# Kernel tuning notes

Hardware: AMD Instinct MI355X
Metric: run time of the kernel (lower is better)

The kernel has to match this reference:

```python
import jax, jax.numpy as jnp
import numpy as np

B, N, D, H, O, A, L = 128, 100, 2048, 1024, 1600, 400, 2048


def _mlp(x, w1, b1, w2, b2, w3, b3):
    h = jax.nn.relu(x @ w1 + b1)
    h = jax.nn.relu(h @ w2 + b2)
    return jax.nn.softmax(h @ w3 + b3, axis=2)  # softmax over class dim (dim=2)


def setup_inputs() -> dict:
    key = jax.random.key(0)
    ks = jax.random.split(key, 18)

    def lin(kw, fan_in, fan_out):
        s = 1.0 / np.sqrt(fan_in)
        return jax.random.normal(kw, (fan_in, fan_out), jnp.float32) * s

    x = jax.random.normal(ks[0], (B, N, D), jnp.float32)
    num_descs = jax.random.randint(ks[1], (B,), 0, N, jnp.int32)
    label_img = jnp.sort(jax.random.randint(ks[2], (L,), 0, B, jnp.int32))
    obj_labels = jax.random.randint(ks[3], (L,), 0, O)
    att_labels = jax.random.randint(ks[4], (L,), 0, A)

    inp = dict(x=x, num_descs=num_descs, label_img=label_img,
               obj_labels=obj_labels, att_labels=att_labels,
               w1o=lin(ks[5], D, H), b1o=jnp.zeros((H,), jnp.float32),
               w2o=lin(ks[6], H, H), b2o=jnp.zeros((H,), jnp.float32),
               w3o=lin(ks[7], H, O), b3o=jnp.zeros((O,), jnp.float32),
               w1a=lin(ks[8], D, H), b1a=jnp.zeros((H,), jnp.float32),
               w2a=lin(ks[9], H, H), b2a=jnp.zeros((H,), jnp.float32),
               w3a=lin(ks[10], H, A), b3a=jnp.zeros((A,), jnp.float32))
    return inp


def reference(x, num_descs, label_img, obj_labels, att_labels,
              w1o, b1o, w2o, b2o, w3o, b3o,
              w1a, b1a, w2a, b2a, w3a, b3a):
    po = _mlp(x, w1o, b1o, w2o, b2o, w3o, b3o)  # [B, N, O]
    pa = _mlp(x, w1a, b1a, w2a, b2a, w3a, b3a)  # [B, N, A]

    rows = jnp.arange(po.shape[1])  # [N]
    # per-label gather of the prob column for its object/attribute class -> [L, N]
    p_obj = po[label_img[:, None], rows[None, :], obj_labels[:, None]]
    p_att = pa[label_img[:, None], rows[None, :], att_labels[:, None]]
    # ragged unpad (descs beyond num_descs[img] excluded from argmax)
    valid = rows[None, :] < num_descs[label_img][:, None]
    score = jnp.where(valid, p_obj * p_att, -jnp.inf)
    desc = jnp.argmax(score, axis=1)  # [L]

    obj_dists = po[label_img, desc, :]  # [L, O]
    att_dists = pa[label_img, desc, :]  # [L, A]
    return (obj_dists, att_dists)
```

## Files before the change

### kernel.cpp

```cpp
#include <hip/hip_runtime.h>
#include <hip/hip_bf16.h>
#include <math.h>

#define Bq 128
#define Nq 100
#define Dq 2048
#define Hq 1024
#define Oq 1600
#define Aq 400
#define Lq 2048
#define Mq (Bq * Nq)
#define OqP 1664
#define AqP 512

typedef __attribute__((ext_vector_type(8))) short bf16x8;
typedef __attribute__((ext_vector_type(16))) float f32x16;
typedef unsigned short ushort;


__device__ __forceinline__ void split1(float v, ushort& h, ushort& l) {
    __hip_bfloat16 bh = __float2bfloat16(v);
    float fh = __bfloat162float(bh);
    __hip_bfloat16 bl = __float2bfloat16(v - fh);
    h = __builtin_bit_cast(ushort, bh);
    l = __builtin_bit_cast(ushort, bl);
}

__device__ __forceinline__ void gl_lds16(const ushort* g, ushort* lds) {
    __builtin_amdgcn_global_load_lds(
        (const __attribute__((address_space(1))) unsigned int*)g,
        (__attribute__((address_space(3))) unsigned int*)lds,
        16, 0, 0);
}

__global__ void build_offsets(const int* __restrict__ num_descs,
                              int* __restrict__ off, int* __restrict__ mc,
                              int* __restrict__ rowmap)
{
    __shared__ int cnt[Bq];
    __shared__ int offs[Bq + 1];
    const int t = threadIdx.x;
    int nd = num_descs[t];
    nd = nd < 0 ? 0 : (nd > Nq ? Nq : nd);
    const int c = nd < 1 ? 1 : nd;
    cnt[t] = c;
    __syncthreads();
    if (t == 0) {
        int s = 0;
        for (int i = 0; i < Bq; i++) { offs[i] = s; s += cnt[i]; }
        offs[Bq] = s;
        mc[0] = s;
        mc[1] = (s + 127) & ~127;
    }
    __syncthreads();
    off[t] = offs[t];
    for (int i = t; i < Mq; i += Bq) rowmap[i] = -1;
    __syncthreads();
    const int o = offs[t];
    for (int n = 0; n < c; n++) rowmap[o + n] = t * Nq + n;
}

__global__ __launch_bounds__(256) void split_compact(const float* __restrict__ x,
                              const int* __restrict__ rowmap,
                              const int* __restrict__ mc,
                              ushort* __restrict__ hi, ushort* __restrict__ lo)
{
    const int KB = Dq / 16;
    const int nbc = Dq / 64;
    const int rt = blockIdx.x / nbc;
    const int bc = (blockIdx.x - rt * nbc) * 64;
    if (rt * 32 >= mc[1]) return;

    __shared__ float t[32][66];
    const int tid = threadIdx.x;
    {
        const int row = tid >> 3;
        const int coff = (tid & 7) * 8;
        const int crow = rt * 32 + row;
        const int orig = (crow < mc[0]) ? rowmap[crow] : -1;
        float v[8];
        if (orig < 0) {
#pragma unroll
            for (int e = 0; e < 8; e++) v[e] = 0.f;
        } else {
            const float* src = x + (size_t)orig * Dq + bc + coff;
            float4 v0 = *(const float4*)(src);
            float4 v1 = *(const float4*)(src + 4);
            v[0] = v0.x; v[1] = v0.y; v[2] = v0.z; v[3] = v0.w;
            v[4] = v1.x; v[5] = v1.y; v[6] = v1.z; v[7] = v1.w;
        }
#pragma unroll
        for (int e = 0; e < 8; e++) t[row][coff + e] = v[e];
    }
    __syncthreads();

    const int wave = tid >> 6;
    const int lane = tid & 63;
    const int r32 = lane & 31;
    const int cl = wave * 16 + (lane >> 5) * 8;
    ushort h[8], l[8];
#pragma unroll
    for (int e = 0; e < 8; e++) split1(t[r32][cl + e], h[e], l[e]);
    const size_t wid = (size_t)rt * KB + (bc >> 4) + wave;
    const size_t a = wid * 512 + (size_t)lane * 8;
    *(bf16x8*)(hi + a) = *(bf16x8*)h;
    *(bf16x8*)(lo + a) = *(bf16x8*)l;
}

struct TSeg { const float* W; ushort* Th; ushort* Tl; int K; int N; int gx; int base; };
struct TSegs { TSeg s[6]; };

__global__ void tsplit_all(TSegs a)
{
    const int id = blockIdx.x;
    TSeg sg = a.s[5];
#pragma unroll
    for (int i = 4; i >= 0; i--) if (id < a.s[i + 1].base) sg = a.s[i];
    const int local = id - sg.base;
    const int bn = (local % sg.gx) * 32;
    const int bk = (local / sg.gx) * 32;
    const int KB = sg.K >> 4;

    __shared__ float t[32][33];
    const int tx = threadIdx.x & 31, ty = threadIdx.x >> 5;
#pragma unroll
    for (int i = 0; i < 4; i++) {
        const int k = bk + ty + i * 8, n = bn + tx;
        t[ty + i * 8][tx] = (n < sg.N) ? sg.W[(size_t)k * sg.N + n] : 0.f;
    }
    __syncthreads();

    const int wave = threadIdx.x >> 6;
    const int lane = threadIdx.x & 63;
    const int kc = wave & 1;
    const int hl = wave >> 1;
    const int nloc = lane & 31;
    const int kloc = kc * 16 + (lane >> 5) * 8;
    ushort v8[8];
#pragma unroll
    for (int e = 0; e < 8; e++) {
        ushort h, l;
        split1(t[kloc + e][nloc], h, l);
        v8[e] = hl ? l : h;
    }
    const size_t chunk = (size_t)((bn >> 5)) * KB + (bk >> 4) + kc;
    ushort* dst = (hl ? sg.Tl : sg.Th) + chunk * 512 + (size_t)lane * 8;
    *(bf16x8*)dst = *(bf16x8*)v8;
}

struct GArgs {
    const ushort* Ah; const ushort* Al;
    const ushort* Bh; const ushort* Bl;
    const float* bias;
    float* Cf; ushort* Ch; ushort* Cl;
    int K, Npad, Nreal, ldc, mode;
};

__global__ __launch_bounds__(256, 3) void gemm_split(GArgs g0, GArgs g1,
                                                     const int* __restrict__ mcp,
                                                     int nct0, int nct)
{
    const int ny = mcp[1] >> 7;
    const int nact = nct * ny;
    const int hw = blockIdx.x;
    if (hw >= nact) return;
    const int q = nact >> 3, r = nact & 7, xcd = hw & 7, pos = hw >> 3;
    const int L = (xcd < r ? xcd * (q + 1) : r * (q + 1) + (xcd - r) * q) + pos;
    const int by = L / nct;
    const int ct = L - by * nct;

    const GArgs g = (ct < nct0) ? g0 : g1;
    const int bm = by * 128;
    const int bn = (ct < nct0 ? ct : ct - nct0) * 128;

    const int KB = g.K >> 4;

    __shared__ __align__(16) ushort sAh[6144];
    __shared__ __align__(16) ushort sAl[6144];
    __shared__ __align__(16) ushort sBh[6144];
    __shared__ __align__(16) ushort sBl[6144];

    const int tid  = threadIdx.x;
    const int wave = tid >> 6;
    const int lane = tid & 63;
    const int wmi = (wave >> 1) * 2;
    const int wni = (wave & 1) * 2;
    const int l31  = lane & 31;
    const int half = lane >> 5;

    const ushort* gAh = g.Ah + ((size_t)(bm / 32 + wave) * KB) * 512 + lane * 8;
    const ushort* gAl = g.Al + ((size_t)(bm / 32 + wave) * KB) * 512 + lane * 8;
    const ushort* gBh = g.Bh + ((size_t)(bn / 32 + wave) * KB) * 512 + lane * 8;
    const ushort* gBl = g.Bl + ((size_t)(bn / 32 + wave) * KB) * 512 + lane * 8;

    f32x16 acc[2][2] = {};

    auto STAGE = [&](int c) {
        const size_t go = (size_t)c * 512;
        const int ls = (c % 3) * 2048 + (wave << 9);
        gl_lds16(gAh + go, &sAh[ls]);
        gl_lds16(gAl + go, &sAl[ls]);
        gl_lds16(gBh + go, &sBh[ls]);
        gl_lds16(gBl + go, &sBl[ls]);
    };

    auto PHASE = [&](int c, int stage_c, int drain) {
        const int slot = (c % 3) * 2048;
        bf16x8 ah[2], al[2], bh[2], bl[2];
#pragma unroll
        for (int i = 0; i < 2; i++) {
            const int sa = slot + (wmi + i) * 512 + lane * 8;
            const int sb = slot + (wni + i) * 512 + lane * 8;
            ah[i] = *(const bf16x8*)&sAh[sa];
            al[i] = *(const bf16x8*)&sAl[sa];
            bh[i] = *(const bf16x8*)&sBh[sb];
            bl[i] = *(const bf16x8*)&sBl[sb];
        }
        if (stage_c >= 0) STAGE(stage_c);
        __builtin_amdgcn_s_setprio(1);
#pragma unroll
        for (int i = 0; i < 2; i++)
#pragma unroll
            for (int j = 0; j < 2; j++) {
                acc[i][j] = __builtin_amdgcn_mfma_f32_32x32x16_bf16(ah[i], bh[j], acc[i][j], 0, 0, 0);
                acc[i][j] = __builtin_amdgcn_mfma_f32_32x32x16_bf16(ah[i], bl[j], acc[i][j], 0, 0, 0);
                acc[i][j] = __builtin_amdgcn_mfma_f32_32x32x16_bf16(al[i], bh[j], acc[i][j], 0, 0, 0);
            }
        __builtin_amdgcn_s_setprio(0);
        if (drain == 4)      asm volatile("s_waitcnt vmcnt(4)" ::: "memory");
        else if (drain == 0) asm volatile("s_waitcnt vmcnt(0)" ::: "memory");
        if (drain >= 0) {
            asm volatile("s_waitcnt lgkmcnt(0)" ::: "memory");
            asm volatile("s_barrier" ::: "memory");
        }
    };

    STAGE(0); STAGE(1);
    asm volatile("s_waitcnt vmcnt(4)" ::: "memory");
    asm volatile("s_barrier" ::: "memory");

    for (int c = 0; c < KB - 2; ++c) PHASE(c, c + 2, 4);
    PHASE(KB - 2, -1, 0);
    PHASE(KB - 1, -1, -1);

    const int KC = g.ldc >> 4;
#pragma unroll
    for (int j = 0; j < 2; j++) {
        const int col = bn + (wni + j) * 32 + l31;
        if (col < g.Nreal) {
            const float bv = g.bias[col];
#pragma unroll
            for (int i = 0; i < 2; i++) {
#pragma unroll
                for (int r = 0; r < 16; r++) {
                    const int row = bm + (wmi + i) * 32 + (r & 3) + 8 * (r >> 2) + 4 * half;
                    float v = acc[i][j][r] + bv;
                    if (g.mode == 1) {
                        v = fmaxf(v, 0.f);
                        ushort h, l;
                        split1(v, h, l);
                        const size_t chunk = (size_t)(row >> 5) * KC + (col >> 4);
                        const size_t adr = chunk * 512
                            + (size_t)((row & 31) + 32 * ((col >> 3) & 1)) * 8 + (col & 7);
                        g.Ch[adr] = h;
                        g.Cl[adr] = l;
                    } else {
                        g.Cf[(size_t)row * g.ldc + col] = v;
                    }
                }
            }
        }
    }
}

__global__ void softmax_stats2(const float* __restrict__ Zo, const float* __restrict__ Za,
                               const int* __restrict__ mc,
                               float* __restrict__ mxo, float* __restrict__ smo,
                               float* __restrict__ mxa, float* __restrict__ sma)
{
    const int r = blockIdx.x;
    if (r >= mc[0]) return;
    const float* Z; int ncols; float* mx; float* sm;
    if (blockIdx.y == 0) { Z = Zo; ncols = Oq; mx = mxo; sm = smo; }
    else                 { Z = Za; ncols = Aq; mx = mxa; sm = sma; }
    const float* row = Z + (size_t)r * ncols;
    __shared__ float red[256];
    float m = -INFINITY;
    for (int c = threadIdx.x; c < ncols; c += 256) m = fmaxf(m, row[c]);
    red[threadIdx.x] = m;
    __syncthreads();
    for (int s = 128; s > 0; s >>= 1) {
        if (threadIdx.x < s) red[threadIdx.x] = fmaxf(red[threadIdx.x], red[threadIdx.x + s]);
        __syncthreads();
    }
    m = red[0];
    __syncthreads();
    float su = 0.f;
    for (int c = threadIdx.x; c < ncols; c += 256) su += expf(row[c] - m);
    red[threadIdx.x] = su;
    __syncthreads();
    for (int s = 128; s > 0; s >>= 1) {
        if (threadIdx.x < s) red[threadIdx.x] += red[threadIdx.x + s];
        __syncthreads();
    }
    if (threadIdx.x == 0) { mx[r] = m; sm[r] = red[0]; }
}

__global__ void argmax_gather(
    const float* __restrict__ Zo, const float* __restrict__ Za,
    const float* __restrict__ mxo, const float* __restrict__ smo,
    const float* __restrict__ mxa, const float* __restrict__ sma,
    const int* __restrict__ label_img, const int* __restrict__ num_descs,
    const int* __restrict__ obj_labels, const int* __restrict__ att_labels,
    const int* __restrict__ off, float* __restrict__ out)
{
    const int l = blockIdx.x;
    const int b = label_img[l];
    const int nd = num_descs[b];
    const int r0 = off[b];
    const int t = threadIdx.x;

    __shared__ float ss[128];
    __shared__ int   si[128];
    if (t < 128) {
        float score = -INFINITY;
        if (t < Nq && t < nd) {
            const int r = r0 + t;
            const float po = expf(Zo[(size_t)r * Oq + obj_labels[l]] - mxo[r]) / smo[r];
            const float pa = expf(Za[(size_t)r * Aq + att_labels[l]] - mxa[r]) / sma[r];
            score = po * pa;
        }
        ss[t] = score;
        si[t] = t;
    }
    __syncthreads();
    for (int s = 64; s > 0; s >>= 1) {
        if (t < s) {
            const float s2 = ss[t + s];
            const int   i2 = si[t + s];
            if (s2 > ss[t] || (s2 == ss[t] && i2 < si[t])) { ss[t] = s2; si[t] = i2; }
        }
        __syncthreads();
    }
    const int r = r0 + si[0];

    const float mo = mxo[r], so = smo[r];
    const float* zo = Zo + (size_t)r * Oq;
    float* oo = out + (size_t)l * Oq;
    for (int c = t; c < Oq; c += 256)
        oo[c] = expf(zo[c] - mo) / so;

    const float ma = mxa[r], sa = sma[r];
    const float* za = Za + (size_t)r * Aq;
    float* oa = out + (size_t)Lq * Oq + (size_t)l * Aq;
    for (int c = t; c < Aq; c += 256)
        oa[c] = expf(za[c] - ma) / sa;
}

extern "C" void kernel_launch(void* const* d_in, const int* in_sizes, int n_in,
                              void* d_out, int out_size, void* d_ws, size_t ws_size,
                              hipStream_t stream)
{
    const float* x          = (const float*)d_in[0];
    const int*   num_descs  = (const int*)d_in[1];
    const int*   label_img  = (const int*)d_in[2];
    const int*   obj_labels = (const int*)d_in[3];
    const int*   att_labels = (const int*)d_in[4];
    const float* w1o = (const float*)d_in[5];  const float* b1o = (const float*)d_in[6];
    const float* w2o = (const float*)d_in[7];  const float* b2o = (const float*)d_in[8];
    const float* w3o = (const float*)d_in[9];  const float* b3o = (const float*)d_in[10];
    const float* w1a = (const float*)d_in[11]; const float* b1a = (const float*)d_in[12];
    const float* w2a = (const float*)d_in[13]; const float* b2a = (const float*)d_in[14];
    const float* w3a = (const float*)d_in[15]; const float* b3a = (const float*)d_in[16];
    float* out = (float*)d_out;

    char* p = (char*)d_ws;
    auto carve = [&](size_t bytes) { char* q = p; p += (bytes + 255) & ~(size_t)255; return q; };

    char* bufA = carve((size_t)Mq * Dq * 2 * 2);
    char* bufB = carve((size_t)Mq * Hq * 2 * 2 * 2);
    ushort* w1oth = (ushort*)carve((size_t)Hq * Dq * 2);  ushort* w1otl = (ushort*)carve((size_t)Hq * Dq * 2);
    ushort* w1ath = (ushort*)carve((size_t)Hq * Dq * 2);  ushort* w1atl = (ushort*)carve((size_t)Hq * Dq * 2);
    ushort* w2oth = (ushort*)carve((size_t)Hq * Hq * 2);  ushort* w2otl = (ushort*)carve((size_t)Hq * Hq * 2);
    ushort* w2ath = (ushort*)carve((size_t)Hq * Hq * 2);  ushort* w2atl = (ushort*)carve((size_t)Hq * Hq * 2);
    ushort* w3oth = (ushort*)carve((size_t)OqP * Hq * 2); ushort* w3otl = (ushort*)carve((size_t)OqP * Hq * 2);
    ushort* w3ath = (ushort*)carve((size_t)AqP * Hq * 2); ushort* w3atl = (ushort*)carve((size_t)AqP * Hq * 2);
    float* mxo = (float*)carve(Mq * 4); float* smo = (float*)carve(Mq * 4);
    float* mxa = (float*)carve(Mq * 4); float* sma = (float*)carve(Mq * 4);
    int* off    = (int*)carve(Bq * 4);
    int* mc     = (int*)carve(4 * 4);
    int* rowmap = (int*)carve(Mq * 4);

    ushort* xh = (ushort*)bufA;
    ushort* xl = xh + (size_t)Mq * Dq;
    ushort* h2oh = (ushort*)bufA;
    ushort* h2ol = h2oh + (size_t)Mq * Hq;
    ushort* h2ah = h2ol + (size_t)Mq * Hq;
    ushort* h2al = h2ah + (size_t)Mq * Hq;
    ushort* h1oh = (ushort*)bufB;
    ushort* h1ol = h1oh + (size_t)Mq * Hq;
    ushort* h1ah = h1ol + (size_t)Mq * Hq;
    ushort* h1al = h1ah + (size_t)Mq * Hq;
    float* z3o = (float*)bufB;
    float* z3a = z3o + (size_t)Mq * Oq;

    build_offsets<<<1, 128, 0, stream>>>(num_descs, off, mc, rowmap);
    split_compact<<<(Mq / 32) * (Dq / 64), 256, 0, stream>>>(x, rowmap, mc, xh, xl);

    {
        TSegs ts;
        int base = 0;
        auto seg = [&](const float* W, ushort* Th, ushort* Tl, int K, int N, int Npad) {
            TSeg s; s.W = W; s.Th = Th; s.Tl = Tl; s.K = K; s.N = N;
            s.gx = Npad / 32; s.base = base; base += (Npad / 32) * (K / 32); return s;
        };
        ts.s[0] = seg(w1o, w1oth, w1otl, Dq, Hq, Hq);
        ts.s[1] = seg(w1a, w1ath, w1atl, Dq, Hq, Hq);
        ts.s[2] = seg(w2o, w2oth, w2otl, Hq, Hq, Hq);
        ts.s[3] = seg(w2a, w2ath, w2atl, Hq, Hq, Hq);
        ts.s[4] = seg(w3o, w3oth, w3otl, Hq, Oq, OqP);
        ts.s[5] = seg(w3a, w3ath, w3atl, Hq, Aq, AqP);
        tsplit_all<<<base, 256, 0, stream>>>(ts);
    }

    {
        GArgs go = { xh, xl, w1oth, w1otl, b1o, nullptr, h1oh, h1ol, Dq, Hq, Hq, Hq, 1 };
        GArgs ga = { xh, xl, w1ath, w1atl, b1a, nullptr, h1ah, h1al, Dq, Hq, Hq, Hq, 1 };
        gemm_split<<<16 * (Mq / 128), 256, 0, stream>>>(go, ga, mc, 8, 16);
    }
    {
        GArgs go = { h1oh, h1ol, w2oth, w2otl, b2o, nullptr, h2oh, h2ol, Hq, Hq, Hq, Hq, 1 };
        GArgs ga = { h1ah, h1al, w2ath, w2atl, b2a, nullptr, h2ah, h2al, Hq, Hq, Hq, Hq, 1 };
        gemm_split<<<16 * (Mq / 128), 256, 0, stream>>>(go, ga, mc, 8, 16);
    }
    {
        GArgs go = { h2oh, h2ol, w3oth, w3otl, b3o, z3o, nullptr, nullptr, Hq, OqP, Oq, Oq, 0 };
        GArgs ga = { h2ah, h2al, w3ath, w3atl, b3a, z3a, nullptr, nullptr, Hq, AqP, Aq, Aq, 0 };
        gemm_split<<<(OqP / 128 + AqP / 128) * (Mq / 128), 256, 0, stream>>>(go, ga, mc,
                                                                            OqP / 128,
                                                                            OqP / 128 + AqP / 128);
    }

    softmax_stats2<<<dim3(Mq, 2), 256, 0, stream>>>(z3o, z3a, mc, mxo, smo, mxa, sma);
    argmax_gather<<<Lq, 256, 0, stream>>>(z3o, z3a, mxo, smo, mxa, sma,
                                          label_img, num_descs, obj_labels, att_labels, off, out);
}
```

Baseline: 638.2 us.

## Enlarge GEMM M-tile to 256 rows with 4x2 MFMA tiles per wave

Doubles the GEMM block tile along M from 128 to 256 rows, so each wave computes a 4x2 grid of 32x32 MFMA tiles and each B tile loaded from memory is reused across twice as many rows. Padding of the compacted row count moves to a 256 multiple, and the staging, wait counts and epilogue are adjusted to match. This cuts global and LDS traffic per FLOP and halves the block count, at the cost of more registers and LDS, lower occupancy (launch bounds 3 to 2), up to 255 padded rows of wasted work, and fewer blocks to spread across CUs.

```diff
diff --git a/kernel.cpp b/kernel.cpp
--- a/kernel.cpp
+++ b/kernel.cpp
@@ -51,6 +51,7 @@
         offs[Bq] = s;
         mc[0] = s;
         mc[1] = (s + 127) & ~127;
+        mc[2] = (s + 255) & ~(int)255;
     }
     __syncthreads();
     off[t] = offs[t];
@@ -69,7 +70,7 @@
     const int nbc = Dq / 64;
     const int rt = blockIdx.x / nbc;
     const int bc = (blockIdx.x - rt * nbc) * 64;
-    if (rt * 32 >= mc[1]) return;
+    if (rt * 32 >= mc[2]) return;
 
     __shared__ float t[32][66];
     const int tid = threadIdx.x;
@@ -156,11 +157,11 @@
     int K, Npad, Nreal, ldc, mode;
 };
 
-__global__ __launch_bounds__(256, 3) void gemm_split(GArgs g0, GArgs g1,
+__global__ __launch_bounds__(256, 2) void gemm_split(GArgs g0, GArgs g1,
                                                      const int* __restrict__ mcp,
                                                      int nct0, int nct)
 {
-    const int ny = mcp[1] >> 7;
+    const int ny = mcp[2] >> 8;
     const int nact = nct * ny;
     const int hw = blockIdx.x;
     if (hw >= nact) return;
@@ -170,56 +171,65 @@
     const int ct = L - by * nct;
 
     const GArgs g = (ct < nct0) ? g0 : g1;
-    const int bm = by * 128;
+    const int bm = by * 256;
     const int bn = (ct < nct0 ? ct : ct - nct0) * 128;
 
     const int KB = g.K >> 4;
 
-    __shared__ __align__(16) ushort sAh[6144];
-    __shared__ __align__(16) ushort sAl[6144];
+    __shared__ __align__(16) ushort sAh[12288];
+    __shared__ __align__(16) ushort sAl[12288];
     __shared__ __align__(16) ushort sBh[6144];
     __shared__ __align__(16) ushort sBl[6144];
 
     const int tid  = threadIdx.x;
     const int wave = tid >> 6;
     const int lane = tid & 63;
-    const int wmi = (wave >> 1) * 2;
-    const int wni = (wave & 1) * 2;
+    const int wm = wave >> 1;
+    const int wn = wave & 1;
     const int l31  = lane & 31;
     const int half = lane >> 5;
 
-    const ushort* gAh = g.Ah + ((size_t)(bm / 32 + wave) * KB) * 512 + lane * 8;
-    const ushort* gAl = g.Al + ((size_t)(bm / 32 + wave) * KB) * 512 + lane * 8;
-    const ushort* gBh = g.Bh + ((size_t)(bn / 32 + wave) * KB) * 512 + lane * 8;
-    const ushort* gBl = g.Bl + ((size_t)(bn / 32 + wave) * KB) * 512 + lane * 8;
-
-    f32x16 acc[2][2] = {};
+    const ushort* gAh0 = g.Ah + ((size_t)(bm / 32 + wave) * KB) * 512 + lane * 8;
+    const ushort* gAh1 = g.Ah + ((size_t)(bm / 32 + wave + 4) * KB) * 512 + lane * 8;
+    const ushort* gAl0 = g.Al + ((size_t)(bm / 32 + wave) * KB) * 512 + lane * 8;
+    const ushort* gAl1 = g.Al + ((size_t)(bm / 32 + wave + 4) * KB) * 512 + lane * 8;
+    const ushort* gBh  = g.Bh + ((size_t)(bn / 32 + wave) * KB) * 512 + lane * 8;
+    const ushort* gBl  = g.Bl + ((size_t)(bn / 32 + wave) * KB) * 512 + lane * 8;
+
+    f32x16 acc[4][2] = {};
 
     auto STAGE = [&](int c) {
         const size_t go = (size_t)c * 512;
-        const int ls = (c % 3) * 2048 + (wave << 9);
-        gl_lds16(gAh + go, &sAh[ls]);
-        gl_lds16(gAl + go, &sAl[ls]);
-        gl_lds16(gBh + go, &sBh[ls]);
-        gl_lds16(gBl + go, &sBl[ls]);
+        const int sa = (c % 3) * 4096;
+        const int sb = (c % 3) * 2048;
+        gl_lds16(gAh0 + go, &sAh[sa + (wave << 9)]);
+        gl_lds16(gAh1 + go, &sAh[sa + ((wave + 4) << 9)]);
+        gl_lds16(gAl0 + go, &sAl[sa + (wave << 9)]);
+        gl_lds16(gAl1 + go, &sAl[sa + ((wave + 4) << 9)]);
+        gl_lds16(gBh + go, &sBh[sb + (wave << 9)]);
+        gl_lds16(gBl + go, &sBl[sb + (wave << 9)]);
     };
 
     auto PHASE = [&](int c, int stage_c, int drain) {
-        const int slot = (c % 3) * 2048;
-        bf16x8 ah[2], al[2], bh[2], bl[2];
-#pragma unroll
-        for (int i = 0; i < 2; i++) {
-            const int sa = slot + (wmi + i) * 512 + lane * 8;
-            const int sb = slot + (wni + i) * 512 + lane * 8;
-            ah[i] = *(const bf16x8*)&sAh[sa];
-            al[i] = *(const bf16x8*)&sAl[sa];
-            bh[i] = *(const bf16x8*)&sBh[sb];
-            bl[i] = *(const bf16x8*)&sBl[sb];
+        const int sa = (c % 3) * 4096;
+        const int sb = (c % 3) * 2048;
+        bf16x8 ah[4], al[4], bh[2], bl[2];
+#pragma unroll
+        for (int i = 0; i < 4; i++) {
+            const int o = sa + (wm * 4 + i) * 512 + lane * 8;
+            ah[i] = *(const bf16x8*)&sAh[o];
+            al[i] = *(const bf16x8*)&sAl[o];
+        }
+#pragma unroll
+        for (int j = 0; j < 2; j++) {
+            const int o = sb + (wn * 2 + j) * 512 + lane * 8;
+            bh[j] = *(const bf16x8*)&sBh[o];
+            bl[j] = *(const bf16x8*)&sBl[o];
         }
         if (stage_c >= 0) STAGE(stage_c);
         __builtin_amdgcn_s_setprio(1);
 #pragma unroll
-        for (int i = 0; i < 2; i++)
+        for (int i = 0; i < 4; i++)
 #pragma unroll
             for (int j = 0; j < 2; j++) {
                 acc[i][j] = __builtin_amdgcn_mfma_f32_32x32x16_bf16(ah[i], bh[j], acc[i][j], 0, 0, 0);
@@ -227,7 +237,7 @@
                 acc[i][j] = __builtin_amdgcn_mfma_f32_32x32x16_bf16(al[i], bh[j], acc[i][j], 0, 0, 0);
             }
         __builtin_amdgcn_s_setprio(0);
-        if (drain == 4)      asm volatile("s_waitcnt vmcnt(4)" ::: "memory");
+        if (drain == 6)      asm volatile("s_waitcnt vmcnt(6)" ::: "memory");
         else if (drain == 0) asm volatile("s_waitcnt vmcnt(0)" ::: "memory");
         if (drain >= 0) {
             asm volatile("s_waitcnt lgkmcnt(0)" ::: "memory");
@@ -236,24 +246,24 @@
     };
 
     STAGE(0); STAGE(1);
-    asm volatile("s_waitcnt vmcnt(4)" ::: "memory");
+    asm volatile("s_waitcnt vmcnt(6)" ::: "memory");
     asm volatile("s_barrier" ::: "memory");
 
-    for (int c = 0; c < KB - 2; ++c) PHASE(c, c + 2, 4);
+    for (int c = 0; c < KB - 2; ++c) PHASE(c, c + 2, 6);
     PHASE(KB - 2, -1, 0);
     PHASE(KB - 1, -1, -1);
 
     const int KC = g.ldc >> 4;
 #pragma unroll
     for (int j = 0; j < 2; j++) {
-        const int col = bn + (wni + j) * 32 + l31;
+        const int col = bn + (wn * 2 + j) * 32 + l31;
         if (col < g.Nreal) {
             const float bv = g.bias[col];
 #pragma unroll
-            for (int i = 0; i < 2; i++) {
+            for (int i = 0; i < 4; i++) {
 #pragma unroll
                 for (int r = 0; r < 16; r++) {
-                    const int row = bm + (wmi + i) * 32 + (r & 3) + 8 * (r >> 2) + 4 * half;
+                    const int row = bm + (wm * 4 + i) * 32 + (r & 3) + 8 * (r >> 2) + 4 * half;
                     float v = acc[i][j][r] + bv;
                     if (g.mode == 1) {
                         v = fmaxf(v, 0.f);
@@ -426,17 +436,17 @@
     {
         GArgs go = { xh, xl, w1oth, w1otl, b1o, nullptr, h1oh, h1ol, Dq, Hq, Hq, Hq, 1 };
         GArgs ga = { xh, xl, w1ath, w1atl, b1a, nullptr, h1ah, h1al, Dq, Hq, Hq, Hq, 1 };
-        gemm_split<<<16 * (Mq / 128), 256, 0, stream>>>(go, ga, mc, 8, 16);
+        gemm_split<<<16 * (Mq / 256), 256, 0, stream>>>(go, ga, mc, 8, 16);
     }
     {
         GArgs go = { h1oh, h1ol, w2oth, w2otl, b2o, nullptr, h2oh, h2ol, Hq, Hq, Hq, Hq, 1 };
         GArgs ga = { h1ah, h1al, w2ath, w2atl, b2a, nullptr, h2ah, h2al, Hq, Hq, Hq, Hq, 1 };
-        gemm_split<<<16 * (Mq / 128), 256, 0, stream>>>(go, ga, mc, 8, 16);
+        gemm_split<<<16 * (Mq / 256), 256, 0, stream>>>(go, ga, mc, 8, 16);
     }
     {
         GArgs go = { h2oh, h2ol, w3oth, w3otl, b3o, z3o, nullptr, nullptr, Hq, OqP, Oq, Oq, 0 };
         GArgs ga = { h2ah, h2al, w3ath, w3atl, b3a, z3a, nullptr, nullptr, Hq, AqP, Aq, Aq, 0 };
-        gemm_split<<<(OqP / 128 + AqP / 128) * (Mq / 128), 256, 0, stream>>>(go, ga, mc,
+        gemm_split<<<(OqP / 128 + AqP / 128) * (Mq / 256), 256, 0, stream>>>(go, ga, mc,
                                                                             OqP / 128,
                                                                             OqP / 128 + AqP / 128);
     }
```

Measured after the change: 546.8 us. 14.3% less time.
